# Optimization experiments

Hardware: AMD Instinct MI355X
Metric: run time of the kernel (lower is better)

The kernel has to match this reference:

```python
import jax, jax.numpy as jnp
import numpy as np

D = 4      # number of tensor modes (leaves of the HT tree)
N = 8      # input dim per mode  (total input  = 8^4 = 4096)
M = 8      # output dim per mode (total output = 8^4 = 4096)
R = 8      # HT rank
B = 512    # batch size
# preorder index of each internal-node core in the stacked `cores` array
CORE_IDX = {(0, 4): 0, (0, 2): 1, (2, 4): 2}


def _contract(a, a_names, b, b_names):
    """tn.contract_between equivalent: contract all shared named axes."""
    shared = [n for n in a_names if n in b_names]
    ax_a = [a_names.index(n) for n in shared]
    ax_b = [b_names.index(n) for n in shared]
    out = jnp.tensordot(a, b, axes=(ax_a, ax_b))
    names = [n for n in a_names if n not in shared] + [n for n in b_names if n not in shared]
    return out, names


def _fwd(x, names, lo, hi, factors, cores):
    """Faithful translation of HTSubTree.forward / build_network.

    Leaf p: factor (in_p, out_p, parent). Internal (lo,hi): core
    (left=parent(lo,mid), right=parent(mid,hi), parent=parent(lo,hi)).
    Contraction order: left subtree, then core, then right subtree; shared
    (pre-connected) edges are contracted automatically, exactly as in
    tn.contract_between on the pre-wired network.
    """
    if hi - lo == 1:
        p = lo
        f_names = [f"in_{p}", f"out_{p}", f"pr_{p}_{p + 1}"]
        return _contract(x, names, factors[p], f_names)
    mid = (lo + hi) // 2
    x, names = _fwd(x, names, lo, mid, factors, cores)
    c_names = [f"pr_{lo}_{mid}", f"pr_{mid}_{hi}", f"pr_{lo}_{hi}"]
    x, names = _contract(x, names, cores[CORE_IDX[(lo, hi)]], c_names)
    return _fwd(x, names, mid, hi, factors, cores)


def setup_inputs() -> dict:
    key = jax.random.key(0)
    k1, k2, k3 = jax.random.split(key, 3)
    x = jax.random.normal(k1, (B, N, N, N, N), dtype=jnp.float32)
    # xavier_normal(fan_in=[in], fan_out=[out, rank]) for factors
    std_f = (2.0 / (N + M * R)) ** 0.5
    factors = jax.random.normal(k2, (D, N, M, R), dtype=jnp.float32) * std_f
    # cores: xavier over rank axes
    std_c = (2.0 / (R + R * R)) ** 0.5
    cores = jax.random.normal(k3, (D - 1, R, R, R), dtype=jnp.float32) * std_c
    return {"x": x, "factors": factors, "cores": cores}


def reference(x, factors, cores):
    names = ["batch"] + [f"in_{p}" for p in range(D)]
    out, names = _fwd(x, names, 0, D, factors, cores)
    # dangling edges: batch, out_0..out_{D-1}, root parent rank -> canonical order
    order = ["batch"] + [f"out_{p}" for p in range(D)] + [f"pr_0_{D}"]
    perm = [names.index(n) for n in order]
    return jnp.transpose(out, perm)  # (B, m0, m1, m2, m3, R)
```

## Files before the change

### kernel.cpp

```cpp
#include <hip/hip_runtime.h>

typedef __attribute__((ext_vector_type(8))) short bf16x8;
typedef __attribute__((ext_vector_type(4))) float f32x4;

static __device__ __forceinline__ short f2bf(float f) {
    union { float f; unsigned u; } v; v.f = f;
    unsigned r = v.u + 0x7fffu + ((v.u >> 16) & 1u);
    return (short)(r >> 16);
}

__global__ __launch_bounds__(256) void ht_pre1(const float* __restrict__ factors,
                                               const float* __restrict__ cores,
                                               short* __restrict__ TLT,
                                               float* __restrict__ TR) {
    int o = (blockIdx.x & 127) * 256 + threadIdx.x;
    if (blockIdx.x < 128) {
        int p = o >> 6, n01 = o & 63;
        int n0 = n01 >> 3, n1 = n01 & 7;
        int mm = p >> 3, r02 = p & 7;
        int m0 = mm >> 3, m1 = mm & 7;
        const float* f0 = factors + n0 * 64 + m0 * 8;
        const float* f1 = factors + 512 + n1 * 64 + m1 * 8;
        const float* c1 = cores + 512;
        float s = 0.f;
        #pragma unroll
        for (int r01 = 0; r01 < 8; ++r01) {
            float a = f0[r01];
            #pragma unroll
            for (int r12 = 0; r12 < 8; ++r12)
                s += a * f1[r12] * c1[r01 * 64 + r12 * 8 + r02];
        }
        TLT[p * 64 + n01] = f2bf(s);
    } else {
        int n23 = o >> 9, m23 = (o >> 3) & 63, r24 = o & 7;
        int n2 = n23 >> 3, n3 = n23 & 7, m2 = m23 >> 3, m3 = m23 & 7;
        const float* f2 = factors + 1024 + n2 * 64 + m2 * 8;
        const float* f3 = factors + 1536 + n3 * 64 + m3 * 8;
        const float* c2 = cores + 1024;
        float s = 0.f;
        #pragma unroll
        for (int r23 = 0; r23 < 8; ++r23) {
            float a = f2[r23];
            #pragma unroll
            for (int r34 = 0; r34 < 8; ++r34)
                s += a * f3[r34] * c2[r23 * 64 + r34 * 8 + r24];
        }
        TR[o] = s;
    }
}

__global__ __launch_bounds__(256) void ht_pre2(const float* __restrict__ cores,
                                               const float* __restrict__ TR,
                                               short* __restrict__ VT) {
    int u = blockIdx.x * 256 + threadIdx.x;
    int base = u * 4;
    int c = base >> 9;
    int k2 = base & 511;
    int m23 = c >> 3, r = c & 7;
    int r02 = k2 >> 6;
    const float* c0 = cores;
    #pragma unroll
    for (int j = 0; j < 4; ++j) {
        int n23 = (k2 + j) & 63;
        float s = 0.f;
        #pragma unroll
        for (int r24 = 0; r24 < 8; ++r24)
            s += TR[n23 * 512 + m23 * 8 + r24] * c0[r02 * 64 + r24 * 8 + r];
        VT[base + j] = f2bf(s);
    }
}

__global__ __launch_bounds__(256, 2) void ht_main(const float* __restrict__ x,
                                                  const short* __restrict__ TLT,
                                                  const short* __restrict__ VT,
                                                  float* __restrict__ out) {
    __shared__ short XT[64 * 64];
    __shared__ short YL[64 * 512];

    const int t = threadIdx.x;
    const int b = blockIdx.x;
    const int w = t >> 6;
    const int l = t & 63;
    const int lr = l & 15;
    const int lk = l >> 4;

    {
        const float* xb = x + b * 4096;
        #pragma unroll
        for (int j = 0; j < 4; ++j) {
            f32x4 v = *(const f32x4*)(xb + j * 1024 + t * 4);
            int n01 = j * 16 + (t >> 4);
            int rbase = (t & 15) * 4;
            #pragma unroll
            for (int e = 0; e < 4; ++e) {
                int rr = rbase + e;
                XT[rr * 64 + (n01 ^ ((rr & 7) << 3))] = f2bf(v[e]);
            }
        }
    }
    __syncthreads();

    {
        bf16x8 bx[4][2];
        #pragma unroll
        for (int ct = 0; ct < 4; ++ct)
            #pragma unroll
            for (int kb = 0; kb < 2; ++kb) {
                int rr = ct * 16 + lr;
                int cc = kb * 32 + lk * 8;
                bx[ct][kb] = *(const bf16x8*)&XT[rr * 64 + (cc ^ ((rr & 7) << 3))];
            }
        #pragma unroll
        for (int pt = 0; pt < 8; ++pt) {
            int pbase = w * 128 + pt * 16;
            const short* arow = TLT + (pbase + lr) * 64;
            bf16x8 a0 = *(const bf16x8*)&arow[lk * 8];
            bf16x8 a1 = *(const bf16x8*)&arow[32 + lk * 8];
            #pragma unroll
            for (int ct = 0; ct < 4; ++ct) {
                f32x4 acc = {0.f, 0.f, 0.f, 0.f};
                acc = __builtin_amdgcn_mfma_f32_16x16x32_bf16(a0, bx[ct][0], acc, 0, 0, 0);
                acc = __builtin_amdgcn_mfma_f32_16x16x32_bf16(a1, bx[ct][1], acc, 0, 0, 0);
                #pragma unroll
                for (int reg = 0; reg < 4; ++reg) {
                    int p = pbase + lk * 4 + reg;
                    int m = p >> 3;
                    int c2 = (p & 7) * 64 + ct * 16 + lr;
                    YL[m * 512 + (c2 ^ ((m & 7) << 3))] = f2bf(acc[reg]);
                }
            }
        }
    }
    __syncthreads();

    {
        f32x4 acc[4][8];
        #pragma unroll
        for (int rt = 0; rt < 4; ++rt)
            #pragma unroll
            for (int ctl = 0; ctl < 8; ++ctl)
                acc[rt][ctl] = (f32x4){0.f, 0.f, 0.f, 0.f};

        for (int kb = 0; kb < 16; ++kb) {
            bf16x8 af[4];
            #pragma unroll
            for (int rt = 0; rt < 4; ++rt) {
                int m = rt * 16 + lr;
                int c2 = kb * 32 + lk * 8;
                af[rt] = *(const bf16x8*)&YL[m * 512 + (c2 ^ ((m & 7) << 3))];
            }
            bf16x8 bfr[8];
            #pragma unroll
            for (int ctl = 0; ctl < 8; ++ctl) {
                int c = (w * 8 + ctl) * 16 + lr;
                bfr[ctl] = *(const bf16x8*)&VT[c * 512 + kb * 32 + lk * 8];
            }
            #pragma unroll
            for (int rt = 0; rt < 4; ++rt)
                #pragma unroll
                for (int ctl = 0; ctl < 8; ++ctl)
                    acc[rt][ctl] = __builtin_amdgcn_mfma_f32_16x16x32_bf16(af[rt], bfr[ctl], acc[rt][ctl], 0, 0, 0);
        }

        float* ob = out + b * 32768;
        #pragma unroll
        for (int rt = 0; rt < 4; ++rt)
            #pragma unroll
            for (int ctl = 0; ctl < 8; ++ctl) {
                int col = (w * 8 + ctl) * 16 + lr;
                #pragma unroll
                for (int reg = 0; reg < 4; ++reg) {
                    int row = rt * 16 + lk * 4 + reg;
                    ob[row * 512 + col] = acc[rt][ctl][reg];
                }
            }
    }
}

extern "C" void kernel_launch(void* const* d_in, const int* in_sizes, int n_in,
                              void* d_out, int out_size, void* d_ws, size_t ws_size,
                              hipStream_t stream) {
    const float* x       = (const float*)d_in[0];
    const float* factors = (const float*)d_in[1];
    const float* cores   = (const float*)d_in[2];
    float* out = (float*)d_out;

    short* TLT = (short*)d_ws;
    short* VT  = TLT + 32768;
    float* TR  = (float*)((char*)d_ws + 65536 + 524288);

    hipLaunchKernelGGL(ht_pre1, dim3(256), dim3(256), 0, stream, factors, cores, TLT, TR);
    hipLaunchKernelGGL(ht_pre2, dim3(256), dim3(256), 0, stream, cores, TR, VT);
    hipLaunchKernelGGL(ht_main, dim3(512), dim3(256), 0, stream, x, TLT, VT, out);
}
```

Baseline: 119.4 us.

## Split main GEMM into staged tiled kernel and fuse precompute kernels

The two precompute kernels are merged into one. The right-subtree intermediate is now kept in shared memory instead of a global buffer, which removes one launch. The main kernel is split in two. The first stage writes the per-batch intermediate Y to a global bf16 buffer. A new tiled GEMM kernel then computes (B*64)x512x512 with 128x128 tiles, double-buffers A through global_load_lds, and uses nontemporal output stores. This improves reuse of VT across batches, since each block previously reloaded all of VT. The cost is an extra round trip of a 32 MB bf16 intermediate through global memory.

```diff
diff --git a/kernel.cpp b/kernel.cpp
--- a/kernel.cpp
+++ b/kernel.cpp
@@ -9,71 +9,90 @@
     return (short)(r >> 16);
 }
 
-__global__ __launch_bounds__(256) void ht_pre1(const float* __restrict__ factors,
-                                               const float* __restrict__ cores,
-                                               short* __restrict__ TLT,
-                                               float* __restrict__ TR) {
-    int o = (blockIdx.x & 127) * 256 + threadIdx.x;
-    if (blockIdx.x < 128) {
-        int p = o >> 6, n01 = o & 63;
-        int n0 = n01 >> 3, n1 = n01 & 7;
-        int mm = p >> 3, r02 = p & 7;
-        int m0 = mm >> 3, m1 = mm & 7;
+__global__ __launch_bounds__(256) void ht_pre(const float* __restrict__ factors,
+                                              const float* __restrict__ cores,
+                                              short* __restrict__ TLT,
+                                              short* __restrict__ VT) {
+    const int bid = blockIdx.x, t = threadIdx.x;
+    if (bid < 64) {
+        __shared__ float TRl[64][9];
+        const int m23 = bid;
+        const int m2 = m23 >> 3, m3 = m23 & 7;
+        {
+            const int v = t * 2;
+            const int n23 = v >> 3;
+            const int r24 = v & 7;
+            const int n2 = n23 >> 3, n3 = n23 & 7;
+            const float* f2p = factors + 1024 + n2 * 64 + m2 * 8;
+            const float* f3p = factors + 1536 + n3 * 64 + m3 * 8;
+            const float* c2p = cores + 1024;
+            float s0 = 0.f, s1 = 0.f;
+            #pragma unroll
+            for (int r23 = 0; r23 < 8; ++r23) {
+                float a = f2p[r23];
+                #pragma unroll
+                for (int r34 = 0; r34 < 8; ++r34) {
+                    float wv = a * f3p[r34];
+                    s0 += wv * c2p[r23 * 64 + r34 * 8 + r24];
+                    s1 += wv * c2p[r23 * 64 + r34 * 8 + r24 + 1];
+                }
+            }
+            TRl[n23][r24] = s0;
+            TRl[n23][r24 + 1] = s1;
+        }
+        __syncthreads();
+        {
+            const int r = t >> 5, seg = t & 31;
+            const int k2b = seg * 16;
+            const int r02 = k2b >> 6;
+            float c0v[8];
+            #pragma unroll
+            for (int r24 = 0; r24 < 8; ++r24)
+                c0v[r24] = cores[r02 * 64 + r24 * 8 + r];
+            short ov[16];
+            #pragma unroll
+            for (int j = 0; j < 16; ++j) {
+                const int n23 = (k2b + j) & 63;
+                float s = 0.f;
+                #pragma unroll
+                for (int r24 = 0; r24 < 8; ++r24)
+                    s += TRl[n23][r24] * c0v[r24];
+                ov[j] = f2bf(s);
+            }
+            short* dst = VT + (m23 * 8 + r) * 512 + k2b;
+            *(bf16x8*)dst = *(bf16x8*)&ov[0];
+            *(bf16x8*)(dst + 8) = *(bf16x8*)&ov[8];
+        }
+    } else {
+        const int idx = ((bid - 64) * 256 + t) * 2;
+        const int p = idx >> 6, n01 = idx & 63;
+        const int n0 = n01 >> 3, n1 = n01 & 7;
+        const int mm = p >> 3, r02 = p & 7;
+        const int m0 = mm >> 3, m1 = mm & 7;
         const float* f0 = factors + n0 * 64 + m0 * 8;
-        const float* f1 = factors + 512 + n1 * 64 + m1 * 8;
+        const float* f1a = factors + 512 + n1 * 64 + m1 * 8;
+        const float* f1b = f1a + 64;
         const float* c1 = cores + 512;
-        float s = 0.f;
+        float s0 = 0.f, s1 = 0.f;
         #pragma unroll
         for (int r01 = 0; r01 < 8; ++r01) {
             float a = f0[r01];
             #pragma unroll
-            for (int r12 = 0; r12 < 8; ++r12)
-                s += a * f1[r12] * c1[r01 * 64 + r12 * 8 + r02];
-        }
-        TLT[p * 64 + n01] = f2bf(s);
-    } else {
-        int n23 = o >> 9, m23 = (o >> 3) & 63, r24 = o & 7;
-        int n2 = n23 >> 3, n3 = n23 & 7, m2 = m23 >> 3, m3 = m23 & 7;
-        const float* f2 = factors + 1024 + n2 * 64 + m2 * 8;
-        const float* f3 = factors + 1536 + n3 * 64 + m3 * 8;
-        const float* c2 = cores + 1024;
-        float s = 0.f;
-        #pragma unroll
-        for (int r23 = 0; r23 < 8; ++r23) {
-            float a = f2[r23];
-            #pragma unroll
-            for (int r34 = 0; r34 < 8; ++r34)
-                s += a * f3[r34] * c2[r23 * 64 + r34 * 8 + r24];
-        }
-        TR[o] = s;
-    }
-}
-
-__global__ __launch_bounds__(256) void ht_pre2(const float* __restrict__ cores,
-                                               const float* __restrict__ TR,
-                                               short* __restrict__ VT) {
-    int u = blockIdx.x * 256 + threadIdx.x;
-    int base = u * 4;
-    int c = base >> 9;
-    int k2 = base & 511;
-    int m23 = c >> 3, r = c & 7;
-    int r02 = k2 >> 6;
-    const float* c0 = cores;
-    #pragma unroll
-    for (int j = 0; j < 4; ++j) {
-        int n23 = (k2 + j) & 63;
-        float s = 0.f;
-        #pragma unroll
-        for (int r24 = 0; r24 < 8; ++r24)
-            s += TR[n23 * 512 + m23 * 8 + r24] * c0[r02 * 64 + r24 * 8 + r];
-        VT[base + j] = f2bf(s);
-    }
-}
-
-__global__ __launch_bounds__(256, 2) void ht_main(const float* __restrict__ x,
-                                                  const short* __restrict__ TLT,
-                                                  const short* __restrict__ VT,
-                                                  float* __restrict__ out) {
+            for (int r12 = 0; r12 < 8; ++r12) {
+                float cv = c1[r01 * 64 + r12 * 8 + r02];
+                s0 += a * f1a[r12] * cv;
+                s1 += a * f1b[r12] * cv;
+            }
+        }
+        unsigned w0 = (unsigned short)f2bf(s0);
+        unsigned w1 = (unsigned short)f2bf(s1);
+        *(unsigned*)&TLT[p * 64 + n01] = w0 | (w1 << 16);
+    }
+}
+
+__global__ __launch_bounds__(256, 2) void ht_g1(const float* __restrict__ x,
+                                                const short* __restrict__ TLT,
+                                                short* __restrict__ A) {
     __shared__ short XT[64 * 64];
     __shared__ short YL[64 * 512];
 
@@ -134,47 +153,85 @@
     __syncthreads();
 
     {
-        f32x4 acc[4][8];
-        #pragma unroll
-        for (int rt = 0; rt < 4; ++rt)
-            #pragma unroll
-            for (int ctl = 0; ctl < 8; ++ctl)
-                acc[rt][ctl] = (f32x4){0.f, 0.f, 0.f, 0.f};
-
-        for (int kb = 0; kb < 16; ++kb) {
-            bf16x8 af[4];
-            #pragma unroll
-            for (int rt = 0; rt < 4; ++rt) {
-                int m = rt * 16 + lr;
-                int c2 = kb * 32 + lk * 8;
-                af[rt] = *(const bf16x8*)&YL[m * 512 + (c2 ^ ((m & 7) << 3))];
-            }
-            bf16x8 bfr[8];
-            #pragma unroll
-            for (int ctl = 0; ctl < 8; ++ctl) {
-                int c = (w * 8 + ctl) * 16 + lr;
-                bfr[ctl] = *(const bf16x8*)&VT[c * 512 + kb * 32 + lk * 8];
-            }
-            #pragma unroll
-            for (int rt = 0; rt < 4; ++rt)
-                #pragma unroll
-                for (int ctl = 0; ctl < 8; ++ctl)
-                    acc[rt][ctl] = __builtin_amdgcn_mfma_f32_16x16x32_bf16(af[rt], bfr[ctl], acc[rt][ctl], 0, 0, 0);
-        }
-
-        float* ob = out + b * 32768;
-        #pragma unroll
-        for (int rt = 0; rt < 4; ++rt)
-            #pragma unroll
-            for (int ctl = 0; ctl < 8; ++ctl) {
-                int col = (w * 8 + ctl) * 16 + lr;
-                #pragma unroll
-                for (int reg = 0; reg < 4; ++reg) {
-                    int row = rt * 16 + lk * 4 + reg;
-                    ob[row * 512 + col] = acc[rt][ctl][reg];
-                }
-            }
-    }
+        short* Ab = A + b * 32768;
+        #pragma unroll
+        for (int it = 0; it < 16; ++it) {
+            int chunk = it * 256 + t;
+            *(bf16x8*)(Ab + chunk * 8) = *(const bf16x8*)(YL + chunk * 8);
+        }
+    }
+}
+
+__global__ __launch_bounds__(256, 4) void ht_g2(const short* __restrict__ A,
+                                                const short* __restrict__ VT,
+                                                float* __restrict__ out) {
+    __shared__ short As[2][128 * 64];
+
+    const int t = threadIdx.x;
+    const int bid = blockIdx.x;
+    const int rt = bid >> 2;
+    const int ct = bid & 3;
+    const int w = t >> 6, l = t & 63;
+    const int lr = l & 15, lk = l >> 4;
+    const int wm = w >> 1, wn = w & 1;
+
+    const short* Ab = A + rt * 65536;
+    const int cbase = ct * 128 + wn * 64;
+
+    f32x4 acc[4][4];
+    #pragma unroll
+    for (int rf = 0; rf < 4; ++rf)
+        #pragma unroll
+        for (int cf = 0; cf < 4; ++cf)
+            acc[rf][cf] = (f32x4){0.f, 0.f, 0.f, 0.f};
+
+    auto stage = [&](int buf, int kb) {
+        #pragma unroll
+        for (int q = 0; q < 4; ++q) {
+            int chunk = q * 256 + t;
+            int row = chunk >> 3, blk = chunk & 7;
+            const short* src = Ab + row * 512 + kb * 64 + blk * 8;
+            __builtin_amdgcn_global_load_lds(
+                (const __attribute__((address_space(1))) unsigned int*)src,
+                (__attribute__((address_space(3))) unsigned int*)&As[buf][chunk * 8],
+                16, 0, 0);
+        }
+    };
+
+    stage(0, 0);
+    __syncthreads();
+
+    for (int kb = 0; kb < 8; ++kb) {
+        const int cur = kb & 1;
+        if (kb < 7) stage(cur ^ 1, kb + 1);
+        #pragma unroll
+        for (int kh = 0; kh < 2; ++kh) {
+            bf16x8 bfr[4];
+            #pragma unroll
+            for (int cf = 0; cf < 4; ++cf)
+                bfr[cf] = *(const bf16x8*)&VT[(cbase + cf * 16 + lr) * 512 + kb * 64 + kh * 32 + lk * 8];
+            #pragma unroll
+            for (int rf = 0; rf < 4; ++rf) {
+                int row = wm * 64 + rf * 16 + lr;
+                int blk = (kh * 4 + lk) ^ (row & 7);
+                bf16x8 af = *(const bf16x8*)&As[cur][row * 64 + blk * 8];
+                #pragma unroll
+                for (int cf = 0; cf < 4; ++cf)
+                    acc[rf][cf] = __builtin_amdgcn_mfma_f32_16x16x32_bf16(af, bfr[cf], acc[rf][cf], 0, 0, 0);
+            }
+        }
+        __syncthreads();
+    }
+
+    float* ob = out + (rt * 128 + wm * 64) * 512 + ct * 128 + wn * 64;
+    #pragma unroll
+    for (int rf = 0; rf < 4; ++rf)
+        #pragma unroll
+        for (int cf = 0; cf < 4; ++cf)
+            #pragma unroll
+            for (int reg = 0; reg < 4; ++reg)
+                __builtin_nontemporal_store(acc[rf][cf][reg],
+                                            &ob[(rf * 16 + lk * 4 + reg) * 512 + cf * 16 + lr]);
 }
 
 extern "C" void kernel_launch(void* const* d_in, const int* in_sizes, int n_in,
@@ -187,9 +244,9 @@
 
     short* TLT = (short*)d_ws;
     short* VT  = TLT + 32768;
-    float* TR  = (float*)((char*)d_ws + 65536 + 524288);
-
-    hipLaunchKernelGGL(ht_pre1, dim3(256), dim3(256), 0, stream, factors, cores, TLT, TR);
-    hipLaunchKernelGGL(ht_pre2, dim3(256), dim3(256), 0, stream, cores, TR, VT);
-    hipLaunchKernelGGL(ht_main, dim3(512), dim3(256), 0, stream, x, TLT, VT, out);
-}
+    short* A   = VT + 262144;
+
+    hipLaunchKernelGGL(ht_pre, dim3(128), dim3(256), 0, stream, factors, cores, TLT, VT);
+    hipLaunchKernelGGL(ht_g1, dim3(512), dim3(256), 0, stream, x, TLT, A);
+    hipLaunchKernelGGL(ht_g2, dim3(1024), dim3(256), 0, stream, A, VT, out);
+}
```

Measured after the change: 133.9 us. 1.12x slower.
